# Performance work log

Hardware: AMD Instinct MI355X
Metric: run time of the kernel (lower is better)

Reference implementation:

```python
import jax, jax.numpy as jnp
import numpy as np

B = 131072
SD, AD, HID = 24, 8, 32
NH = SD + AD            # n_heads = 32
UNITS = HID * NH        # 1024


def _xavier(k, shape):
    fan_in, fan_out = shape[-2], shape[-1]
    lim = float(np.sqrt(6.0 / (fan_in + fan_out)))
    return jax.random.uniform(k, shape, jnp.float32, -lim, lim)


def setup_inputs() -> dict:
    key = jax.random.key(0)
    ks = jax.random.split(key, 8)
    return dict(
        state=jax.random.normal(ks[0], (B, SD), jnp.float32),
        action=jax.random.normal(ks[1], (B, AD), jnp.float32),
        # ripple layer 1: per-head Linear(NH -> HID), gate logits init 0 (init_prob=0.5)
        W1=_xavier(ks[2], (NH, NH, HID)), b1=jnp.zeros((NH, HID), jnp.float32), g1=jnp.zeros((NH,), jnp.float32),
        # ripple layer 2: per-head Linear(UNITS -> HID)
        W2=_xavier(ks[3], (NH, UNITS, HID)), b2=jnp.zeros((NH, HID), jnp.float32), g2=jnp.zeros((NH,), jnp.float32),
        # q_network
        Wq1=_xavier(ks[4], (UNITS, 256)), bq1=jnp.zeros((256,), jnp.float32),
        ln1_g=jnp.ones((256,), jnp.float32), ln1_b=jnp.zeros((256,), jnp.float32),
        Wq2=_xavier(ks[5], (256, 128)), bq2=jnp.zeros((128,), jnp.float32),
        ln2_g=jnp.ones((128,), jnp.float32), ln2_b=jnp.zeros((128,), jnp.float32),
        Wq3=_xavier(ks[6], (128, 1)), bq3=jnp.zeros((1,), jnp.float32),
    )


def _ripple(x, W, b, g):
    # x: [B, D]; W: [H, D, K]; per-head linear + tanh, scaled by per-head sigmoid gate
    h = jnp.tanh(jnp.einsum('bd,hdk->bhk', x, W) + b[None])  # [B, H, K]
    h = h * jax.nn.sigmoid(g)[None, :, None]
    return h.reshape(x.shape[0], -1)  # [B, H*K]


def _ln(x, g, b, eps=1e-5):
    mu = jnp.mean(x, -1, keepdims=True)
    var = jnp.mean((x - mu) ** 2, -1, keepdims=True)
    return (x - mu) * jax.lax.rsqrt(var + eps) * g + b


def reference(state, action, W1, b1, g1, W2, b2, g2,
              Wq1, bq1, ln1_g, ln1_b, Wq2, bq2, ln2_g, ln2_b, Wq3, bq3):
    sa = jnp.concatenate([state, action], axis=1)          # [B, SD+AD]
    x = _ripple(sa, W1, b1, g1)                            # [B, UNITS]
    x = _ripple(x, W2, b2, g2)                             # [B, UNITS]
    h = jax.nn.relu(_ln(x @ Wq1 + bq1, ln1_g, ln1_b))      # [B, 256] (dropout = eval identity)
    h = jax.nn.relu(_ln(h @ Wq2 + bq2, ln2_g, ln2_b))      # [B, 128]
    return h @ Wq3 + bq3                                   # [B, 1]
```

## Files before the change

### kernel.cpp

```cpp
#include <hip/hip_runtime.h>
#include <hip/hip_bf16.h>

typedef _Float16 f16x8 __attribute__((ext_vector_type(8)));
typedef _Float16 f16x4 __attribute__((ext_vector_type(4)));
typedef float f32x4 __attribute__((ext_vector_type(4)));

__device__ __forceinline__ float tanh_fast(float x) {
  float e = __expf(2.0f * x);
  return 1.0f - 2.0f * __builtin_amdgcn_rcpf(e + 1.0f);
}
__device__ __forceinline__ float sigmoid_fast(float x) {
  return __builtin_amdgcn_rcpf(1.0f + __expf(-x));
}

__global__ __launch_bounds__(256) void prep_weights(
    const float* __restrict__ W1, const float* __restrict__ W2,
    const float* __restrict__ Wq1, const float* __restrict__ Wq2,
    _Float16* __restrict__ V1p, _Float16* __restrict__ V2p,
    _Float16* __restrict__ T1p, _Float16* __restrict__ T2p) {
  __shared__ float S[32 * 33];
  int b = blockIdx.x, t = threadIdx.x;
  if (b < 2624) {
    const float* in; _Float16* out; int N, nc0, tile, use_pi;
    if (b < 2048) {
      int h = b >> 6, rem = b & 63, ntl = rem >> 5, kt = rem & 31;
      in = W2 + (size_t)h * 32768 + (size_t)kt * 32 * 32;
      N = 32; nc0 = ntl * 16;
      out = V2p; tile = kt * 64 + (h * 2 + ntl); use_pi = 1;
    } else if (b < 2560) {
      int i = b - 2048, nt = i >> 5, kt = i & 31;
      in = Wq1 + (size_t)kt * 32 * 256; N = 256; nc0 = nt * 16;
      out = T1p; tile = kt * 16 + nt; use_pi = 1;
    } else {
      int i = b - 2560, nt = i >> 3, kt = i & 7;
      in = Wq2 + (size_t)kt * 32 * 128; N = 128; nc0 = nt * 16;
      out = T2p; tile = nt * 8 + kt; use_pi = 0;
    }
    if (t < 128) {
      int r = t >> 2, c4 = (t & 3) * 4;
      const float4 v = *(const float4*)(in + (size_t)r * N + nc0 + c4);
      S[r * 17 + c4 + 0] = v.x; S[r * 17 + c4 + 1] = v.y;
      S[r * 17 + c4 + 2] = v.z; S[r * 17 + c4 + 3] = v.w;
    }
    __syncthreads();
    if (t < 128) {
      int w2 = t >> 6, l = t & 63, q = l >> 4, l15 = l & 15;
      f16x4 o;
#pragma unroll
      for (int jj = 0; jj < 4; ++jj) {
        int kl = use_pi ? (q * 4 + jj + w2 * 16) : (q * 8 + w2 * 4 + jj);
        o[jj] = (_Float16)S[kl * 17 + l15];
      }
      *(f16x4*)(out + (size_t)tile * 512 + l * 8 + w2 * 4) = o;
    }
  } else {
    int h = b - 2624;
    const float* in = W1 + h * 1024;
    int cc = t & 31, rr8 = t >> 5;
#pragma unroll
    for (int p = 0; p < 4; ++p) {
      int r = rr8 + p * 8;
      S[cc * 33 + r] = in[r * 32 + cc];
    }
    __syncthreads();
    if (t < 128) {
      int ntl = t >> 6, l = t & 63, q = l >> 4, l15 = l & 15;
      f16x8 o;
#pragma unroll
      for (int j = 0; j < 8; ++j)
        o[j] = (_Float16)S[(ntl * 16 + l15) * 33 + q * 8 + j];
      *(f16x8*)(V1p + (size_t)(h * 2 + ntl) * 512 + l * 8) = o;
    }
  }
}

__global__ __launch_bounds__(512, 2) void k12q(
    const float* __restrict__ state, const float* __restrict__ action,
    const _Float16* __restrict__ v1p, const float* __restrict__ b1,
    const float* __restrict__ g1,
    const _Float16* __restrict__ v2p, const float* __restrict__ b2,
    const float* __restrict__ g2,
    const _Float16* __restrict__ t1p, const _Float16* __restrict__ t2p,
    const float* __restrict__ bq1, const float* __restrict__ ln1g,
    const float* __restrict__ ln1b,
    const float* __restrict__ bq2, const float* __restrict__ ln2g,
    const float* __restrict__ ln2b,
    const float* __restrict__ wq3, const float* __restrict__ bq3,
    float* __restrict__ out) {
  __shared__ __align__(16) _Float16 LB[65536];
  __shared__ float redA[64 * 8], redB[64 * 8];
  __shared__ float meanv[64], rstdv[64];
  _Float16* SA  = LB;
  _Float16* XBb = LB + 2560;
  _Float16* x2h = LB;
  _Float16* y1h = LB;

  int bm = blockIdx.x;
  int t = threadIdx.x, w = t >> 6, l = t & 63, q = l >> 4, l15 = l & 15;
  int m0 = bm * 64;

  {
    int r = t >> 3, qq = t & 7;
    size_t grow = (size_t)(m0 + r);
    const float* src = (qq < 6) ? (state + grow * 24 + qq * 4)
                                : (action + grow * 8 + (qq - 6) * 4);
    float4 v = *(const float4*)src;
    f16x4 h;
    h[0] = (_Float16)v.x; h[1] = (_Float16)v.y;
    h[2] = (_Float16)v.z; h[3] = (_Float16)v.w;
    *(f16x4*)&SA[r * 40 + qq * 4] = h;
  }
  __syncthreads();

  f16x8 asa[4];
#pragma unroll
  for (int p = 0; p < 4; ++p)
    asa[p] = *(const f16x8*)&SA[(p * 16 + l15) * 40 + q * 8];

  const int nt0 = w * 8;
  const _Float16* bBase = v2p + (size_t)nt0 * 512 + (size_t)l * 8;
  f32x4 acc[4][8] = {};

  auto produce = [&](int h, int buf) {
    f16x8 rb0 = *(const f16x8*)(v1p + (size_t)(2 * h) * 512 + l * 8);
    f16x8 rb1 = *(const f16x8*)(v1p + (size_t)(2 * h + 1) * 512 + l * 8);
    float sg = sigmoid_fast(g1[h]);
    f32x4 bs0 = *(const f32x4*)(b1 + h * 32 + q * 4);
    f32x4 bs1 = *(const f32x4*)(b1 + h * 32 + 16 + q * 4);
    _Float16* bw = XBb + (size_t)buf * 16384 + (size_t)((h & 7) * 4) * 512 + l * 8;
#pragma unroll
    for (int pp = 0; pp < 4; ++pp) {
      f32x4 d0 = {}, d1 = {};
      d0 = __builtin_amdgcn_mfma_f32_16x16x32_f16(rb0, asa[pp], d0, 0, 0, 0);
      d1 = __builtin_amdgcn_mfma_f32_16x16x32_f16(rb1, asa[pp], d1, 0, 0, 0);
      f16x8 o;
#pragma unroll
      for (int r = 0; r < 4; ++r) {
        o[r]     = (_Float16)(tanh_fast(d0[r] + bs0[r]) * sg);
        o[4 + r] = (_Float16)(tanh_fast(d1[r] + bs1[r]) * sg);
      }
      *(f16x8*)(bw + (size_t)pp * 512) = o;
    }
  };

  f16x8 bb0[4], bb1v[4];
#pragma unroll
  for (int n2 = 0; n2 < 4; ++n2)
    bb0[n2] = *(const f16x8*)(bBase + (size_t)n2 * 512);
#pragma unroll
  for (int n2 = 0; n2 < 4; ++n2)
    bb1v[n2] = *(const f16x8*)(bBase + (size_t)(4 + n2) * 512);
  produce(w, 0);
  __syncthreads();

  f16x8 xab[2][4];
#pragma unroll
  for (int p = 0; p < 4; ++p) {
    const _Float16* buf = XBb + (size_t)(p & 1) * 16384;
#pragma unroll
    for (int mi = 0; mi < 4; ++mi)
      xab[0][mi] = *(const f16x8*)(buf + (size_t)mi * 512 + l * 8);
#pragma unroll
    for (int ktl = 0; ktl < 8; ++ktl) {
      int kt = p * 8 + ktl;
      if (ktl == w && p < 3) produce((p + 1) * 8 + w, (p & 1) ^ 1);
      if (ktl < 7) {
#pragma unroll
        for (int mi = 0; mi < 4; ++mi)
          xab[(ktl + 1) & 1][mi] =
              *(const f16x8*)(buf + (size_t)((ktl + 1) * 4 + mi) * 512 + l * 8);
      }
      __builtin_amdgcn_s_setprio(1);
#pragma unroll
      for (int mi = 0; mi < 4; ++mi)
#pragma unroll
        for (int n2 = 0; n2 < 4; ++n2)
          acc[mi][n2] = __builtin_amdgcn_mfma_f32_16x16x32_f16(
              bb0[n2], xab[ktl & 1][mi], acc[mi][n2], 0, 0, 0);
      if (kt < 31) {
#pragma unroll
        for (int n2 = 0; n2 < 4; ++n2)
          bb0[n2] = *(const f16x8*)(bBase + (size_t)((kt + 1) * 64 + n2) * 512);
      }
#pragma unroll
      for (int mi = 0; mi < 4; ++mi)
#pragma unroll
        for (int n2 = 0; n2 < 4; ++n2)
          acc[mi][4 + n2] = __builtin_amdgcn_mfma_f32_16x16x32_f16(
              bb1v[n2], xab[ktl & 1][mi], acc[mi][4 + n2], 0, 0, 0);
      if (kt < 31) {
#pragma unroll
        for (int n2 = 0; n2 < 4; ++n2)
          bb1v[n2] = *(const f16x8*)(bBase + (size_t)((kt + 1) * 64 + 4 + n2) * 512);
      }
      __builtin_amdgcn_s_setprio(0);
    }
    if (p < 3) __syncthreads();
  }

  __syncthreads();

#pragma unroll
  for (int mi = 0; mi < 4; ++mi)
#pragma unroll
    for (int p2 = 0; p2 < 4; ++p2) {
      int kc2 = w * 4 + p2;
      float sg2 = sigmoid_fast(g2[kc2]);
      f32x4 c0 = *(const f32x4*)(b2 + kc2 * 32 + q * 4);
      f32x4 c1 = *(const f32x4*)(b2 + kc2 * 32 + 16 + q * 4);
      f16x8 o;
#pragma unroll
      for (int r = 0; r < 4; ++r) {
        o[r]     = (_Float16)(tanh_fast(acc[mi][2 * p2][r] + c0[r]) * sg2);
        o[4 + r] = (_Float16)(tanh_fast(acc[mi][2 * p2 + 1][r] + c1[r]) * sg2);
      }
      *(f16x8*)(x2h + (size_t)(kc2 * 4 + mi) * 512 + l * 8) = o;
    }
  __syncthreads();

  f32x4 acc2[4][2] = {};
  {
    f16x8 aC[4], aN[4], bf0C, bf1C, bf0N, bf1N;
#pragma unroll
    for (int mi = 0; mi < 4; ++mi)
      aC[mi] = *(const f16x8*)(x2h + (size_t)mi * 512 + l * 8);
    bf0C = *(const f16x8*)(t1p + (size_t)(w * 2) * 512 + l * 8);
    bf1C = *(const f16x8*)(t1p + (size_t)(w * 2 + 1) * 512 + l * 8);
#pragma unroll
    for (int kt = 0; kt < 32; ++kt) {
      if (kt < 31) {
#pragma unroll
        for (int mi = 0; mi < 4; ++mi)
          aN[mi] = *(const f16x8*)(x2h + (size_t)((kt + 1) * 4 + mi) * 512 + l * 8);
        bf0N = *(const f16x8*)(t1p + (size_t)((kt + 1) * 16 + w * 2) * 512 + l * 8);
        bf1N = *(const f16x8*)(t1p + (size_t)((kt + 1) * 16 + w * 2 + 1) * 512 + l * 8);
      }
#pragma unroll
      for (int mi = 0; mi < 4; ++mi) {
        acc2[mi][0] = __builtin_amdgcn_mfma_f32_16x16x32_f16(aC[mi], bf0C, acc2[mi][0], 0, 0, 0);
        acc2[mi][1] = __builtin_amdgcn_mfma_f32_16x16x32_f16(aC[mi], bf1C, acc2[mi][1], 0, 0, 0);
      }
#pragma unroll
      for (int mi = 0; mi < 4; ++mi) aC[mi] = aN[mi];
      bf0C = bf0N; bf1C = bf1N;
    }
  }

#pragma unroll
  for (int ni = 0; ni < 2; ++ni) {
    int col = w * 32 + ni * 16 + l15;
    float b = bq1[col];
#pragma unroll
    for (int mi = 0; mi < 4; ++mi)
#pragma unroll
      for (int r = 0; r < 4; ++r) acc2[mi][ni][r] += b;
  }
#pragma unroll
  for (int mi = 0; mi < 4; ++mi)
#pragma unroll
    for (int r = 0; r < 4; ++r) {
      int row = mi * 16 + q * 4 + r;
      float s = 0.f, sq = 0.f;
#pragma unroll
      for (int ni = 0; ni < 2; ++ni) { float v = acc2[mi][ni][r]; s += v; sq += v * v; }
#pragma unroll
      for (int off = 1; off < 16; off <<= 1) { s += __shfl_xor(s, off); sq += __shfl_xor(sq, off); }
      if (l15 == 0) { redA[row * 8 + w] = s; redB[row * 8 + w] = sq; }
    }
  __syncthreads();
  if (t < 64) {
    float s = 0.f, sq = 0.f;
#pragma unroll
    for (int i = 0; i < 8; ++i) { s += redA[t * 8 + i]; sq += redB[t * 8 + i]; }
    float mean = s * (1.0f / 256.0f);
    float var = sq * (1.0f / 256.0f) - mean * mean;
    meanv[t] = mean; rstdv[t] = rsqrtf(var + 1e-5f);
  }
  __syncthreads();
#pragma unroll
  for (int mi = 0; mi < 4; ++mi)
#pragma unroll
    for (int ni = 0; ni < 2; ++ni)
#pragma unroll
      for (int r = 0; r < 4; ++r) {
        int row = mi * 16 + q * 4 + r;
        int col = w * 32 + ni * 16 + l15;
        float y = (acc2[mi][ni][r] - meanv[row]) * rstdv[row] * ln1g[col] + ln1b[col];
        y = fmaxf(y, 0.f);
        y1h[row * 264 + col] = (_Float16)y;
      }
  __syncthreads();

  f32x4 a3[4] = {};
  for (int kt = 0; kt < 8; ++kt) {
    f16x8 af[4];
#pragma unroll
    for (int mi = 0; mi < 4; ++mi)
      af[mi] = *(const f16x8*)&y1h[(mi * 16 + l15) * 264 + kt * 32 + q * 8];
    f16x8 bf = *(const f16x8*)(t2p + (size_t)(w * 8 + kt) * 512 + l * 8);
#pragma unroll
    for (int mi = 0; mi < 4; ++mi)
      a3[mi] = __builtin_amdgcn_mfma_f32_16x16x32_f16(af[mi], bf, a3[mi], 0, 0, 0);
  }
  {
    int col = w * 16 + l15;
    float b = bq2[col];
#pragma unroll
    for (int mi = 0; mi < 4; ++mi)
#pragma unroll
      for (int r = 0; r < 4; ++r) a3[mi][r] += b;
  }
  __syncthreads();
#pragma unroll
  for (int mi = 0; mi < 4; ++mi)
#pragma unroll
    for (int r = 0; r < 4; ++r) {
      int row = mi * 16 + q * 4 + r;
      float s = a3[mi][r], sq = s * s;
#pragma unroll
      for (int off = 1; off < 16; off <<= 1) { s += __shfl_xor(s, off); sq += __shfl_xor(sq, off); }
      if (l15 == 0) { redA[row * 8 + w] = s; redB[row * 8 + w] = sq; }
    }
  __syncthreads();
  if (t < 64) {
    float s = 0.f, sq = 0.f;
#pragma unroll
    for (int i = 0; i < 8; ++i) { s += redA[t * 8 + i]; sq += redB[t * 8 + i]; }
    float mean = s * (1.0f / 128.0f);
    float var = sq * (1.0f / 128.0f) - mean * mean;
    meanv[t] = mean; rstdv[t] = rsqrtf(var + 1e-5f);
  }
  __syncthreads();
#pragma unroll
  for (int mi = 0; mi < 4; ++mi)
#pragma unroll
    for (int r = 0; r < 4; ++r) {
      int row = mi * 16 + q * 4 + r;
      int col = w * 16 + l15;
      float y = (a3[mi][r] - meanv[row]) * rstdv[row] * ln2g[col] + ln2b[col];
      y = fmaxf(y, 0.f);
      float pr = y * wq3[col];
#pragma unroll
      for (int off = 1; off < 16; off <<= 1) pr += __shfl_xor(pr, off);
      if (l15 == 0) redA[row * 8 + w] = pr;
    }
  __syncthreads();
  if (t < 64) {
    float s = 0.f;
#pragma unroll
    for (int i = 0; i < 8; ++i) s += redA[t * 8 + i];
    out[m0 + t] = s + bq3[0];
  }
}

extern "C" void kernel_launch(void* const* d_in, const int* in_sizes, int n_in,
                              void* d_out, int out_size, void* d_ws, size_t ws_size,
                              hipStream_t stream) {
  const float* state  = (const float*)d_in[0];
  const float* action = (const float*)d_in[1];
  const float* W1  = (const float*)d_in[2];
  const float* b1  = (const float*)d_in[3];
  const float* g1  = (const float*)d_in[4];
  const float* W2  = (const float*)d_in[5];
  const float* b2  = (const float*)d_in[6];
  const float* g2  = (const float*)d_in[7];
  const float* Wq1 = (const float*)d_in[8];
  const float* bq1 = (const float*)d_in[9];
  const float* ln1g = (const float*)d_in[10];
  const float* ln1b = (const float*)d_in[11];
  const float* Wq2 = (const float*)d_in[12];
  const float* bq2 = (const float*)d_in[13];
  const float* ln2g = (const float*)d_in[14];
  const float* ln2b = (const float*)d_in[15];
  const float* Wq3 = (const float*)d_in[16];
  const float* bq3 = (const float*)d_in[17];
  int B = in_sizes[0] / 24;

  char* ws = (char*)d_ws;
  _Float16* V1p = (_Float16*)(ws);
  _Float16* V2p = (_Float16*)(ws + 65536);
  _Float16* T1p = (_Float16*)(ws + 65536 + 2097152);
  _Float16* T2p = (_Float16*)(ws + 65536 + 2097152 + 524288);

  prep_weights<<<2656, 256, 0, stream>>>(W1, W2, Wq1, Wq2, V1p, V2p, T1p, T2p);

  int nb = B / 64;
  k12q<<<dim3(nb), 512, 0, stream>>>(state, action, V1p, b1, g1,
                                     V2p, b2, g2, T1p, T2p,
                                     bq1, ln1g, ln1b, bq2, ln2g, ln2b,
                                     Wq3, bq3, (float*)d_out);
}
```

Baseline: 600.2 us.

## Split layer-1 producer into halves and drop register double-buffering of X tiles

The layer-1 ripple producer is split into two half-head calls, one per 16-column MFMA output, issued at different k-steps so each wave's tanh/MFMA work is spread more evenly across the layer-2 main loop. The register double-buffer of the X A-fragments is replaced by loading the current tile at the top of each iteration, which lowers register pressure but exposes LDS latency. The LDS row pitch of the y1h buffer also changes from 264 to 268 halves to alter bank mapping. That pitch is no longer a multiple of 16 bytes for the f16x8 reads and may exceed the original allocation, which risks misaligned LDS accesses or an overflow.

```diff
diff --git a/kernel.cpp b/kernel.cpp
--- a/kernel.cpp
+++ b/kernel.cpp
@@ -121,25 +121,20 @@
   const _Float16* bBase = v2p + (size_t)nt0 * 512 + (size_t)l * 8;
   f32x4 acc[4][8] = {};
 
-  auto produce = [&](int h, int buf) {
-    f16x8 rb0 = *(const f16x8*)(v1p + (size_t)(2 * h) * 512 + l * 8);
-    f16x8 rb1 = *(const f16x8*)(v1p + (size_t)(2 * h + 1) * 512 + l * 8);
+  auto produceHalf = [&](int h, int buf, int e) {
+    f16x8 rb = *(const f16x8*)(v1p + (size_t)(2 * h + e) * 512 + l * 8);
     float sg = sigmoid_fast(g1[h]);
-    f32x4 bs0 = *(const f32x4*)(b1 + h * 32 + q * 4);
-    f32x4 bs1 = *(const f32x4*)(b1 + h * 32 + 16 + q * 4);
-    _Float16* bw = XBb + (size_t)buf * 16384 + (size_t)((h & 7) * 4) * 512 + l * 8;
+    f32x4 bs = *(const f32x4*)(b1 + h * 32 + e * 16 + q * 4);
+    _Float16* bw = XBb + (size_t)buf * 16384 + (size_t)((h & 7) * 4) * 512 + l * 8 + e * 4;
 #pragma unroll
     for (int pp = 0; pp < 4; ++pp) {
-      f32x4 d0 = {}, d1 = {};
-      d0 = __builtin_amdgcn_mfma_f32_16x16x32_f16(rb0, asa[pp], d0, 0, 0, 0);
-      d1 = __builtin_amdgcn_mfma_f32_16x16x32_f16(rb1, asa[pp], d1, 0, 0, 0);
-      f16x8 o;
-#pragma unroll
-      for (int r = 0; r < 4; ++r) {
-        o[r]     = (_Float16)(tanh_fast(d0[r] + bs0[r]) * sg);
-        o[4 + r] = (_Float16)(tanh_fast(d1[r] + bs1[r]) * sg);
-      }
-      *(f16x8*)(bw + (size_t)pp * 512) = o;
+      f32x4 d = {};
+      d = __builtin_amdgcn_mfma_f32_16x16x32_f16(rb, asa[pp], d, 0, 0, 0);
+      f16x4 o;
+#pragma unroll
+      for (int r = 0; r < 4; ++r)
+        o[r] = (_Float16)(tanh_fast(d[r] + bs[r]) * sg);
+      *(f16x4*)(bw + (size_t)pp * 512) = o;
     }
   };
 
@@ -150,33 +145,29 @@
 #pragma unroll
   for (int n2 = 0; n2 < 4; ++n2)
     bb1v[n2] = *(const f16x8*)(bBase + (size_t)(4 + n2) * 512);
-  produce(w, 0);
-  __syncthreads();
-
-  f16x8 xab[2][4];
+  produceHalf(w, 0, 0);
+  produceHalf(w, 0, 1);
+  __syncthreads();
+
 #pragma unroll
   for (int p = 0; p < 4; ++p) {
     const _Float16* buf = XBb + (size_t)(p & 1) * 16384;
 #pragma unroll
-    for (int mi = 0; mi < 4; ++mi)
-      xab[0][mi] = *(const f16x8*)(buf + (size_t)mi * 512 + l * 8);
-#pragma unroll
     for (int ktl = 0; ktl < 8; ++ktl) {
       int kt = p * 8 + ktl;
-      if (ktl == w && p < 3) produce((p + 1) * 8 + w, (p & 1) ^ 1);
-      if (ktl < 7) {
-#pragma unroll
-        for (int mi = 0; mi < 4; ++mi)
-          xab[(ktl + 1) & 1][mi] =
-              *(const f16x8*)(buf + (size_t)((ktl + 1) * 4 + mi) * 512 + l * 8);
-      }
+      f16x8 xa[4];
+#pragma unroll
+      for (int mi = 0; mi < 4; ++mi)
+        xa[mi] = *(const f16x8*)(buf + (size_t)(ktl * 4 + mi) * 512 + l * 8);
+      if (ktl == w && p < 3) produceHalf((p + 1) * 8 + w, (p & 1) ^ 1, 0);
+      if (ktl == ((w + 4) & 7) && p < 3) produceHalf((p + 1) * 8 + w, (p & 1) ^ 1, 1);
       __builtin_amdgcn_s_setprio(1);
 #pragma unroll
       for (int mi = 0; mi < 4; ++mi)
 #pragma unroll
         for (int n2 = 0; n2 < 4; ++n2)
           acc[mi][n2] = __builtin_amdgcn_mfma_f32_16x16x32_f16(
-              bb0[n2], xab[ktl & 1][mi], acc[mi][n2], 0, 0, 0);
+              bb0[n2], xa[mi], acc[mi][n2], 0, 0, 0);
       if (kt < 31) {
 #pragma unroll
         for (int n2 = 0; n2 < 4; ++n2)
@@ -187,7 +178,7 @@
 #pragma unroll
         for (int n2 = 0; n2 < 4; ++n2)
           acc[mi][4 + n2] = __builtin_amdgcn_mfma_f32_16x16x32_f16(
-              bb1v[n2], xab[ktl & 1][mi], acc[mi][4 + n2], 0, 0, 0);
+              bb1v[n2], xa[mi], acc[mi][4 + n2], 0, 0, 0);
       if (kt < 31) {
 #pragma unroll
         for (int n2 = 0; n2 < 4; ++n2)
@@ -287,7 +278,7 @@
         int col = w * 32 + ni * 16 + l15;
         float y = (acc2[mi][ni][r] - meanv[row]) * rstdv[row] * ln1g[col] + ln1b[col];
         y = fmaxf(y, 0.f);
-        y1h[row * 264 + col] = (_Float16)y;
+        y1h[row * 268 + col] = (_Float16)y;
       }
   __syncthreads();
 
@@ -296,7 +287,7 @@
     f16x8 af[4];
 #pragma unroll
     for (int mi = 0; mi < 4; ++mi)
-      af[mi] = *(const f16x8*)&y1h[(mi * 16 + l15) * 264 + kt * 32 + q * 8];
+      af[mi] = *(const f16x8*)&y1h[(mi * 16 + l15) * 268 + kt * 32 + q * 8];
     f16x8 bf = *(const f16x8*)(t2p + (size_t)(w * 8 + kt) * 512 + l * 8);
 #pragma unroll
     for (int mi = 0; mi < 4; ++mi)
```

Result: slower. 649.7 us (+8.2%).

## Split fused kernel into ripple and q-head kernels via chunked global staging

Applied to the files above, without the earlier changes.

Splits the single fused kernel into two kernels. The first computes both ripple layers and writes the fp16 layer-2 activations to a workspace buffer in MFMA tile layout. The second reads them back for the q-network and layer norms. Rows are processed in chunks sized to the workspace. The first kernel's layer-1 production is restructured into two 16-head halves with deeper staging and without setprio. The split lets each kernel tune its own LDS use and occupancy, but adds a global round-trip of activations and more launches.

```diff
diff --git a/kernel.cpp b/kernel.cpp
--- a/kernel.cpp
+++ b/kernel.cpp
@@ -74,34 +74,22 @@
   }
 }
 
-__global__ __launch_bounds__(512, 2) void k12q(
+__global__ __launch_bounds__(512, 2) void k12_fused(
     const float* __restrict__ state, const float* __restrict__ action,
     const _Float16* __restrict__ v1p, const float* __restrict__ b1,
     const float* __restrict__ g1,
     const _Float16* __restrict__ v2p, const float* __restrict__ b2,
     const float* __restrict__ g2,
-    const _Float16* __restrict__ t1p, const _Float16* __restrict__ t2p,
-    const float* __restrict__ bq1, const float* __restrict__ ln1g,
-    const float* __restrict__ ln1b,
-    const float* __restrict__ bq2, const float* __restrict__ ln2g,
-    const float* __restrict__ ln2b,
-    const float* __restrict__ wq3, const float* __restrict__ bq3,
-    float* __restrict__ out) {
-  __shared__ __align__(16) _Float16 LB[65536];
-  __shared__ float redA[64 * 8], redB[64 * 8];
-  __shared__ float meanv[64], rstdv[64];
-  _Float16* SA  = LB;
-  _Float16* XBb = LB + 2560;
-  _Float16* x2h = LB;
-  _Float16* y1h = LB;
-
+    _Float16* __restrict__ x2p, int gro, int NRT) {
+  __shared__ __align__(16) _Float16 SA[64 * 40];
+  __shared__ __align__(16) _Float16 XB[2][16 * 4 * 512];
   int bm = blockIdx.x;
   int t = threadIdx.x, w = t >> 6, l = t & 63, q = l >> 4, l15 = l & 15;
   int m0 = bm * 64;
 
   {
     int r = t >> 3, qq = t & 7;
-    size_t grow = (size_t)(m0 + r);
+    size_t grow = (size_t)(gro + m0 + r);
     const float* src = (qq < 6) ? (state + grow * 24 + qq * 4)
                                 : (action + grow * 8 + (qq - 6) * 4);
     float4 v = *(const float4*)src;
@@ -127,19 +115,19 @@
     float sg = sigmoid_fast(g1[h]);
     f32x4 bs0 = *(const f32x4*)(b1 + h * 32 + q * 4);
     f32x4 bs1 = *(const f32x4*)(b1 + h * 32 + 16 + q * 4);
-    _Float16* bw = XBb + (size_t)buf * 16384 + (size_t)((h & 7) * 4) * 512 + l * 8;
-#pragma unroll
-    for (int pp = 0; pp < 4; ++pp) {
+    _Float16* bw = &XB[buf][(size_t)((h & 15) * 4) * 512 + l * 8];
+#pragma unroll
+    for (int p = 0; p < 4; ++p) {
       f32x4 d0 = {}, d1 = {};
-      d0 = __builtin_amdgcn_mfma_f32_16x16x32_f16(rb0, asa[pp], d0, 0, 0, 0);
-      d1 = __builtin_amdgcn_mfma_f32_16x16x32_f16(rb1, asa[pp], d1, 0, 0, 0);
+      d0 = __builtin_amdgcn_mfma_f32_16x16x32_f16(rb0, asa[p], d0, 0, 0, 0);
+      d1 = __builtin_amdgcn_mfma_f32_16x16x32_f16(rb1, asa[p], d1, 0, 0, 0);
       f16x8 o;
 #pragma unroll
       for (int r = 0; r < 4; ++r) {
         o[r]     = (_Float16)(tanh_fast(d0[r] + bs0[r]) * sg);
         o[4 + r] = (_Float16)(tanh_fast(d1[r] + bs1[r]) * sg);
       }
-      *(f16x8*)(bw + (size_t)pp * 512) = o;
+      *(f16x8*)(bw + (size_t)p * 512) = o;
     }
   };
 
@@ -150,61 +138,90 @@
 #pragma unroll
   for (int n2 = 0; n2 < 4; ++n2)
     bb1v[n2] = *(const f16x8*)(bBase + (size_t)(4 + n2) * 512);
-  produce(w, 0);
+  produce(w * 2, 0);
+  produce(w * 2 + 1, 0);
   __syncthreads();
 
   f16x8 xab[2][4];
 #pragma unroll
-  for (int p = 0; p < 4; ++p) {
-    const _Float16* buf = XBb + (size_t)(p & 1) * 16384;
-#pragma unroll
-    for (int mi = 0; mi < 4; ++mi)
-      xab[0][mi] = *(const f16x8*)(buf + (size_t)mi * 512 + l * 8);
-#pragma unroll
-    for (int ktl = 0; ktl < 8; ++ktl) {
-      int kt = p * 8 + ktl;
-      if (ktl == w && p < 3) produce((p + 1) * 8 + w, (p & 1) ^ 1);
-      if (ktl < 7) {
-#pragma unroll
-        for (int mi = 0; mi < 4; ++mi)
-          xab[(ktl + 1) & 1][mi] =
-              *(const f16x8*)(buf + (size_t)((ktl + 1) * 4 + mi) * 512 + l * 8);
-      }
-      __builtin_amdgcn_s_setprio(1);
+  for (int mi = 0; mi < 4; ++mi)
+    xab[0][mi] = *(const f16x8*)&XB[0][(size_t)mi * 512 + l * 8];
+
+#pragma unroll
+  for (int ktl = 0; ktl < 16; ++ktl) {
+    int kt = ktl;
+    if (ktl == 6)  produce(16 + w * 2, 1);
+    if (ktl == 10) produce(16 + w * 2 + 1, 1);
+    if (ktl < 15) {
 #pragma unroll
       for (int mi = 0; mi < 4; ++mi)
-#pragma unroll
-        for (int n2 = 0; n2 < 4; ++n2)
-          acc[mi][n2] = __builtin_amdgcn_mfma_f32_16x16x32_f16(
-              bb0[n2], xab[ktl & 1][mi], acc[mi][n2], 0, 0, 0);
-      if (kt < 31) {
-#pragma unroll
-        for (int n2 = 0; n2 < 4; ++n2)
-          bb0[n2] = *(const f16x8*)(bBase + (size_t)((kt + 1) * 64 + n2) * 512);
-      }
+        xab[(ktl + 1) & 1][mi] =
+            *(const f16x8*)&XB[0][(size_t)((ktl + 1) * 4 + mi) * 512 + l * 8];
+    }
+#pragma unroll
+    for (int mi = 0; mi < 4; ++mi)
+#pragma unroll
+      for (int n2 = 0; n2 < 4; ++n2)
+        acc[mi][n2] = __builtin_amdgcn_mfma_f32_16x16x32_f16(
+            bb0[n2], xab[ktl & 1][mi], acc[mi][n2], 0, 0, 0);
+#pragma unroll
+    for (int n2 = 0; n2 < 4; ++n2)
+      bb0[n2] = *(const f16x8*)(bBase + (size_t)((kt + 1) * 64 + n2) * 512);
+#pragma unroll
+    for (int mi = 0; mi < 4; ++mi)
+#pragma unroll
+      for (int n2 = 0; n2 < 4; ++n2)
+        acc[mi][4 + n2] = __builtin_amdgcn_mfma_f32_16x16x32_f16(
+            bb1v[n2], xab[ktl & 1][mi], acc[mi][4 + n2], 0, 0, 0);
+#pragma unroll
+    for (int n2 = 0; n2 < 4; ++n2)
+      bb1v[n2] = *(const f16x8*)(bBase + (size_t)((kt + 1) * 64 + 4 + n2) * 512);
+  }
+  __syncthreads();
+
+#pragma unroll
+  for (int mi = 0; mi < 4; ++mi)
+    xab[0][mi] = *(const f16x8*)&XB[1][(size_t)mi * 512 + l * 8];
+
+#pragma unroll
+  for (int ktl = 0; ktl < 16; ++ktl) {
+    int kt = 16 + ktl;
+    if (ktl < 15) {
 #pragma unroll
       for (int mi = 0; mi < 4; ++mi)
-#pragma unroll
-        for (int n2 = 0; n2 < 4; ++n2)
-          acc[mi][4 + n2] = __builtin_amdgcn_mfma_f32_16x16x32_f16(
-              bb1v[n2], xab[ktl & 1][mi], acc[mi][4 + n2], 0, 0, 0);
-      if (kt < 31) {
-#pragma unroll
-        for (int n2 = 0; n2 < 4; ++n2)
-          bb1v[n2] = *(const f16x8*)(bBase + (size_t)((kt + 1) * 64 + 4 + n2) * 512);
-      }
-      __builtin_amdgcn_s_setprio(0);
-    }
-    if (p < 3) __syncthreads();
-  }
-
-  __syncthreads();
-
-#pragma unroll
-  for (int mi = 0; mi < 4; ++mi)
+        xab[(ktl + 1) & 1][mi] =
+            *(const f16x8*)&XB[1][(size_t)((ktl + 1) * 4 + mi) * 512 + l * 8];
+    }
+#pragma unroll
+    for (int mi = 0; mi < 4; ++mi)
+#pragma unroll
+      for (int n2 = 0; n2 < 4; ++n2)
+        acc[mi][n2] = __builtin_amdgcn_mfma_f32_16x16x32_f16(
+            bb0[n2], xab[ktl & 1][mi], acc[mi][n2], 0, 0, 0);
+    if (kt < 31) {
+#pragma unroll
+      for (int n2 = 0; n2 < 4; ++n2)
+        bb0[n2] = *(const f16x8*)(bBase + (size_t)((kt + 1) * 64 + n2) * 512);
+    }
+#pragma unroll
+    for (int mi = 0; mi < 4; ++mi)
+#pragma unroll
+      for (int n2 = 0; n2 < 4; ++n2)
+        acc[mi][4 + n2] = __builtin_amdgcn_mfma_f32_16x16x32_f16(
+            bb1v[n2], xab[ktl & 1][mi], acc[mi][4 + n2], 0, 0, 0);
+    if (kt < 31) {
+#pragma unroll
+      for (int n2 = 0; n2 < 4; ++n2)
+        bb1v[n2] = *(const f16x8*)(bBase + (size_t)((kt + 1) * 64 + 4 + n2) * 512);
+    }
+  }
+
+#pragma unroll
+  for (int mi = 0; mi < 4; ++mi) {
+    int rt = bm * 4 + mi;
 #pragma unroll
     for (int p2 = 0; p2 < 4; ++p2) {
-      int kc2 = w * 4 + p2;
+      int kc2 = (nt0 >> 1) + p2;
       float sg2 = sigmoid_fast(g2[kc2]);
       f32x4 c0 = *(const f32x4*)(b2 + kc2 * 32 + q * 4);
       f32x4 c1 = *(const f32x4*)(b2 + kc2 * 32 + 16 + q * 4);
@@ -214,16 +231,35 @@
         o[r]     = (_Float16)(tanh_fast(acc[mi][2 * p2][r] + c0[r]) * sg2);
         o[4 + r] = (_Float16)(tanh_fast(acc[mi][2 * p2 + 1][r] + c1[r]) * sg2);
       }
-      *(f16x8*)(x2h + (size_t)(kc2 * 4 + mi) * 512 + l * 8) = o;
-    }
-  __syncthreads();
+      *(f16x8*)(x2p + ((size_t)kc2 * NRT + rt) * 512 + l * 8) = o;
+    }
+  }
+}
+
+__global__ __launch_bounds__(512, 3) void k3_head64(
+    const _Float16* __restrict__ x2p, const _Float16* __restrict__ t1p,
+    const _Float16* __restrict__ t2p,
+    const float* __restrict__ bq1, const float* __restrict__ ln1g,
+    const float* __restrict__ ln1b,
+    const float* __restrict__ bq2, const float* __restrict__ ln2g,
+    const float* __restrict__ ln2b,
+    const float* __restrict__ wq3, const float* __restrict__ bq3,
+    float* __restrict__ out, int NRT) {
+  __shared__ __align__(16) _Float16 y1h[64 * 268];
+  __shared__ float redA[64 * 8], redB[64 * 8];
+  __shared__ float meanv[64], rstdv[64];
+  int bm = blockIdx.x;
+  int t = threadIdx.x, w = t >> 6, l = t & 63, q = l >> 4, l15 = l & 15;
+  int rt0 = bm * 4;
 
   f32x4 acc2[4][2] = {};
   {
+    const _Float16* aBase = x2p + (size_t)rt0 * 512 + (size_t)l * 8;
+    const size_t aK = (size_t)NRT * 512;
     f16x8 aC[4], aN[4], bf0C, bf1C, bf0N, bf1N;
 #pragma unroll
     for (int mi = 0; mi < 4; ++mi)
-      aC[mi] = *(const f16x8*)(x2h + (size_t)mi * 512 + l * 8);
+      aC[mi] = *(const f16x8*)(aBase + (size_t)mi * 512);
     bf0C = *(const f16x8*)(t1p + (size_t)(w * 2) * 512 + l * 8);
     bf1C = *(const f16x8*)(t1p + (size_t)(w * 2 + 1) * 512 + l * 8);
 #pragma unroll
@@ -231,7 +267,7 @@
       if (kt < 31) {
 #pragma unroll
         for (int mi = 0; mi < 4; ++mi)
-          aN[mi] = *(const f16x8*)(x2h + (size_t)((kt + 1) * 4 + mi) * 512 + l * 8);
+          aN[mi] = *(const f16x8*)(aBase + (size_t)(kt + 1) * aK + (size_t)mi * 512);
         bf0N = *(const f16x8*)(t1p + (size_t)((kt + 1) * 16 + w * 2) * 512 + l * 8);
         bf1N = *(const f16x8*)(t1p + (size_t)((kt + 1) * 16 + w * 2 + 1) * 512 + l * 8);
       }
@@ -287,7 +323,7 @@
         int col = w * 32 + ni * 16 + l15;
         float y = (acc2[mi][ni][r] - meanv[row]) * rstdv[row] * ln1g[col] + ln1b[col];
         y = fmaxf(y, 0.f);
-        y1h[row * 264 + col] = (_Float16)y;
+        y1h[row * 268 + col] = (_Float16)y;
       }
   __syncthreads();
 
@@ -296,7 +332,7 @@
     f16x8 af[4];
 #pragma unroll
     for (int mi = 0; mi < 4; ++mi)
-      af[mi] = *(const f16x8*)&y1h[(mi * 16 + l15) * 264 + kt * 32 + q * 8];
+      af[mi] = *(const f16x8*)&y1h[(mi * 16 + l15) * 268 + kt * 32 + q * 8];
     f16x8 bf = *(const f16x8*)(t2p + (size_t)(w * 8 + kt) * 512 + l * 8);
 #pragma unroll
     for (int mi = 0; mi < 4; ++mi)
@@ -349,7 +385,7 @@
     float s = 0.f;
 #pragma unroll
     for (int i = 0; i < 8; ++i) s += redA[t * 8 + i];
-    out[m0 + t] = s + bq3[0];
+    out[bm * 64 + t] = s + bq3[0];
   }
 }
 
@@ -381,12 +417,25 @@
   _Float16* V2p = (_Float16*)(ws + 65536);
   _Float16* T1p = (_Float16*)(ws + 65536 + 2097152);
   _Float16* T2p = (_Float16*)(ws + 65536 + 2097152 + 524288);
+  size_t woff = (65536 + 2097152 + 524288 + 65536 + 4095) & ~(size_t)4095;
+
+  size_t avail = ws_size > woff ? ws_size - woff : 0;
+  long rows = (long)(avail / 2048);
+  if (rows > 32768) rows = 32768;
+  rows &= ~127L;
+  if (rows < 128) rows = 128;
+  int S = (int)rows;
+  _Float16* x2 = (_Float16*)(ws + woff);
+  int NRT = S / 16;
 
   prep_weights<<<2656, 256, 0, stream>>>(W1, W2, Wq1, Wq2, V1p, V2p, T1p, T2p);
 
-  int nb = B / 64;
-  k12q<<<dim3(nb), 512, 0, stream>>>(state, action, V1p, b1, g1,
-                                     V2p, b2, g2, T1p, T2p,
-                                     bq1, ln1g, ln1b, bq2, ln2g, ln2b,
-                                     Wq3, bq3, (float*)d_out);
-}
+  for (int r0 = 0; r0 < B; r0 += S) {
+    int Sc = S < (B - r0) ? S : (B - r0);
+    k12_fused<<<dim3(Sc / 64), 512, 0, stream>>>(state, action, V1p, b1, g1,
+                                                 V2p, b2, g2, x2, r0, NRT);
+    k3_head64<<<dim3(Sc / 64), 512, 0, stream>>>(x2, T1p, T2p, bq1, ln1g, ln1b,
+                                                 bq2, ln2g, ln2b, Wq3, bq3,
+                                                 (float*)d_out + r0, NRT);
+  }
+}
```

New measurement: 615.9 us. 2.6% more time.
